# Performance work log

Hardware: AMD Instinct MI355X
Metric: run time of the kernel (lower is better)

## Reference

```python
import jax, jax.numpy as jnp
import numpy as np

B, N_HEADS, F_TOK = 8, 12, 768
GRID_H, GRID_W = 32, 32
N_TOK = 1 + GRID_H * GRID_W  # 1025 (readout token + patches)
F_HEAD = F_TOK // N_HEADS    # 64
NUM_DIST = (2 * GRID_H - 1) * (2 * GRID_W - 1) + 3  # 3972


def _build_relpos_index(gh, gw):
    # BEiT-style relative position index with 3 extra slots for the readout token
    coords = np.stack(np.meshgrid(np.arange(gh), np.arange(gw), indexing='ij'))  # (2, gh, gw)
    flat = coords.reshape(2, -1)                                                 # (2, gh*gw)
    rel = flat[:, :, None] - flat[:, None, :]                                    # (2, P, P)
    rel = rel.transpose(1, 2, 0).astype(np.int64)                                # (P, P, 2)
    rel[:, :, 0] += gh - 1
    rel[:, :, 1] += gw - 1
    rel[:, :, 0] *= 2 * gw - 1
    rpi = rel.sum(-1)                                                            # (P, P)
    n = 1 + gh * gw
    nd = (2 * gh - 1) * (2 * gw - 1) + 3
    idx = np.zeros((n, n), dtype=np.int32)
    idx[1:, 1:] = rpi
    idx[0, :] = nd - 3  # readout -> all
    idx[:, 0] = nd - 2  # all -> readout
    idx[0, 0] = nd - 1  # readout -> readout
    return idx


def setup_inputs() -> dict:
    key = jax.random.key(0)
    ks = jax.random.split(key, 7)
    tokens = jax.random.normal(ks[0], (B, N_TOK, F_TOK), dtype=jnp.float32)
    qkv_w = jax.random.normal(ks[1], (3 * F_TOK, F_TOK), dtype=jnp.float32) * 0.02
    q_bias = jax.random.normal(ks[2], (1, N_HEADS, 1, F_HEAD), dtype=jnp.float32) * 0.02
    v_bias = jax.random.normal(ks[3], (1, N_HEADS, 1, F_HEAD), dtype=jnp.float32) * 0.02
    relpos_table = jax.random.normal(ks[4], (NUM_DIST, N_HEADS), dtype=jnp.float32) * 0.02
    proj_w = jax.random.normal(ks[5], (F_TOK, F_TOK), dtype=jnp.float32) * 0.02
    proj_b = jax.random.normal(ks[6], (F_TOK,), dtype=jnp.float32) * 0.02
    relpos_index = jnp.asarray(_build_relpos_index(GRID_H, GRID_W))  # (N, N) int32
    return {
        'tokens': tokens, 'qkv_w': qkv_w, 'q_bias': q_bias, 'v_bias': v_bias,
        'relpos_table': relpos_table, 'proj_w': proj_w, 'proj_b': proj_b,
        'relpos_index': relpos_index, 'patch_h': GRID_H, 'patch_w': GRID_W,
    }


def reference(tokens, qkv_w, q_bias, v_bias, relpos_table, proj_w, proj_b,
              relpos_index, patch_h, patch_w):
    b, n, f_tok = tokens.shape
    # qkv projection (no bias): (B, N, 3F) -> (3, B, H, N, f)
    qkv = tokens @ qkv_w.T
    qkv = qkv.reshape(b, n, 3, N_HEADS, F_HEAD).transpose(2, 0, 3, 1, 4)
    q, k, v = qkv[0], qkv[1], qkv[2]
    q = (q + q_bias) * (F_HEAD ** -0.5)
    v = v + v_bias
    # attention scores: (B, H, N, N)
    attn = jnp.einsum('bhnf,bhmf->bhnm', q, k)
    # relative position bias gather: (N, N, H) -> (H, N, N)
    bias = relpos_table[relpos_index].transpose(2, 0, 1)
    attn = attn + bias[None]
    w = jax.nn.softmax(attn, axis=-1)
    out = jnp.einsum('bhnm,bhmf->bhnf', w, v)
    out = out.transpose(0, 2, 1, 3).reshape(b, n, N_HEADS * F_HEAD)
    return out @ proj_w.T + proj_b
```

## Files before the change

### kernel.cpp

```cpp
#include <hip/hip_runtime.h>

#define B_ 8
#define NH 12
#define NTOK 1025
#define FT 768
#define MROWS (B_*NTOK)
#define QPAD 1025
#define CH2 34
#define NQT 36
#define NTT 34
#define NRT18 18
#define NDIST 3972
#define LOG2E 1.44269504089f

typedef __bf16 bf16x8 __attribute__((ext_vector_type(8)));
typedef __bf16 bf16x2 __attribute__((ext_vector_type(2)));
typedef float floatx4 __attribute__((ext_vector_type(4)));
typedef float floatx16 __attribute__((ext_vector_type(16)));
typedef int intx4 __attribute__((ext_vector_type(4)));

__device__ __forceinline__ void async_ld16(const void* gp, void* lp) {
  __builtin_amdgcn_global_load_lds(
      (const __attribute__((address_space(1))) void*)gp,
      (__attribute__((address_space(3))) void*)lp, 16, 0, 0);
}

__global__ __launch_bounds__(256) void cvt_bf16(const float* __restrict__ src,
                                                __bf16* __restrict__ dst, int n4) {
  int i = blockIdx.x * 256 + threadIdx.x;
  if (i >= n4) return;
  float4 v = ((const float4*)src)[i];
  __bf16 o[4] = {(__bf16)v.x, (__bf16)v.y, (__bf16)v.z, (__bf16)v.w};
  *(uint2*)(dst + 4 * (size_t)i) = *(uint2*)o;
}

__global__ __launch_bounds__(256) void table_prep(const float* __restrict__ table,
                                                  __bf16* __restrict__ tableT) {
  int i = blockIdx.x * 256 + threadIdx.x;
  if (i >= NH * NDIST) return;
  int h = i / NDIST, d = i - h * NDIST;
  tableT[i] = (__bf16)(table[(size_t)d * NH + h] * LOG2E);
}

__global__ __launch_bounds__(256) void bias_gather_t(
    const int* __restrict__ idx, const __bf16* __restrict__ tableT,
    __bf16* __restrict__ Bb) {
  __shared__ int ids_l[32][33];
  const int qt = blockIdx.x, tt = blockIdx.y;
  const int t = threadIdx.x;
  {
    const int row = t >> 3, c4 = (t & 7) * 4;
    int qrow = qt * 32 + row; if (qrow > NTOK - 1) qrow = NTOK - 1;
    const int* src = idx + (size_t)qrow * NTOK;
#pragma unroll
    for (int j = 0; j < 4; ++j) {
      int token = tt * 32 + c4 + j; if (token > NTOK - 1) token = NTOK - 1;
      ids_l[row][c4 + j] = src[token];
    }
  }
  __syncthreads();
  const int lane = t & 63, w = t >> 6;
  const int l31 = lane & 31, hb = lane >> 5;
  int ids[16]; bool ok[16];
#pragma unroll
  for (int j = 0; j < 16; ++j) {
    const int col = (j & 3) + 8 * (j >> 2) + 4 * hb;
    ok[j] = tt * 32 + col < NTOK;
    ids[j] = ids_l[l31][col];
  }
#pragma unroll
  for (int g = 0; g < 3; ++g) {
    const int h = w + g * 4;
    const __bf16* tb = tableT + (size_t)h * NDIST;
    __bf16 v[16] __attribute__((aligned(16)));
#pragma unroll
    for (int j = 0; j < 16; ++j)
      v[j] = ok[j] ? tb[ids[j]] : (__bf16)(-1e30f);
    uint4* dst = (uint4*)(Bb + (((size_t)h * NQT + qt) * NTT + tt) * 1024 + lane * 16);
    dst[0] = ((uint4*)v)[0];
    dst[1] = ((uint4*)v)[1];
  }
}

__device__ __forceinline__ void gemm128_pipe(
    const __bf16* __restrict__ A, const __bf16* __restrict__ W,
    int am0, int n0, int amax, __bf16* At, __bf16* Bt, floatx4 acc[4][4]) {
  const int tid = threadIdx.x, wave = tid >> 6, lane = tid & 63;
  const int l = lane & 15, qd = lane >> 4;
  const int wr = wave >> 1, wc = wave & 1;
  const int srow = lane >> 2, sg = lane & 3;
  const int r0 = wave * 32 + srow, r1 = r0 + 16;
  int gm0 = am0 + r0; if (gm0 > amax) gm0 = amax;
  int gm1 = am0 + r1; if (gm1 > amax) gm1 = amax;
  const int sw0 = (sg ^ (r0 & 3)) * 8;
  const __bf16* gA0 = A + (size_t)gm0 * FT + sw0;
  const __bf16* gA1 = A + (size_t)gm1 * FT + sw0;
  const __bf16* gB0 = W + (size_t)(n0 + r0) * FT + sw0;
  const __bf16* gB1 = W + (size_t)(n0 + r1) * FT + sw0;
  const int woff = wave * 32 * 32;
  const int fsw = (qd ^ (l & 3)) * 8;

  auto issue = [&](int k, int buf) {
    __bf16* a = At + buf * 4096 + woff;
    __bf16* b = Bt + buf * 4096 + woff;
    async_ld16(gA0 + k * 32, a);
    async_ld16(gA1 + k * 32, a + 512);
    async_ld16(gB0 + k * 32, b);
    async_ld16(gB1 + k * 32, b + 512);
  };
  auto step = [&](int buf) {
    __builtin_amdgcn_s_barrier();
    const __bf16* ab = At + buf * 4096;
    const __bf16* bb = Bt + buf * 4096;
    bf16x8 aF[4], bF[4];
#pragma unroll
    for (int t = 0; t < 4; ++t)
      aF[t] = *(const bf16x8*)(ab + (wr * 64 + t * 16 + l) * 32 + fsw);
#pragma unroll
    for (int u = 0; u < 4; ++u)
      bF[u] = *(const bf16x8*)(bb + (wc * 64 + u * 16 + l) * 32 + fsw);
#pragma unroll
    for (int t = 0; t < 4; ++t)
#pragma unroll
      for (int u = 0; u < 4; ++u)
        acc[t][u] = __builtin_amdgcn_mfma_f32_16x16x32_bf16(aF[t], bF[u], acc[t][u], 0, 0, 0);
  };

  issue(0, 0);
  issue(1, 1);
  for (int k = 0; k < 24; ++k) {
    if (k + 2 < 24) {
      issue(k + 2, (k + 2) & 3);
      __builtin_amdgcn_s_waitcnt(0x0F78);
    } else if (k + 1 < 24) {
      __builtin_amdgcn_s_waitcnt(0x0F74);
    } else {
      __builtin_amdgcn_s_waitcnt(0x0F70);
    }
    step(k & 3);
  }
}

__global__ __launch_bounds__(256) void qkv_gemm128(
    const __bf16* __restrict__ tokens, const __bf16* __restrict__ qkvw,
    const float* __restrict__ qbias, const float* __restrict__ vbias,
    __bf16* __restrict__ Qb, __bf16* __restrict__ Kc, __bf16* __restrict__ Vc) {
  __shared__ __bf16 At[4 * 4096], Bt[4 * 4096];
  const int u0 = blockIdx.x;
  const int c = u0 & 7, q0 = u0 >> 3;
  const int mt = (q0 / 18) * 8 + c, ni = q0 % 18;
  const int b = mt / 9, ml = mt - b * 9;
  const int am0 = b * NTOK + ml * 128, amax = b * NTOK + 1024;
  const int n0 = ni * 128;
  const int tid = threadIdx.x, wave = tid >> 6, lane = tid & 63;
  const int l = lane & 15, qd = lane >> 4;
  const int wr = wave >> 1, wc = wave & 1;
  floatx4 acc[4][4];
#pragma unroll
  for (int t = 0; t < 4; ++t)
#pragma unroll
    for (int u = 0; u < 4; ++u) acc[t][u] = (floatx4){0.f, 0.f, 0.f, 0.f};
  gemm128_pipe(tokens, qkvw, am0, n0, amax, At, Bt, acc);

  const int which = ni / 6;
  const int nrem0 = (ni - which * 6) * 128;
  const bool full = (ml < 8);
  const int tokb = ml * 128 + wr * 64 + qd * 4;

  if (which == 0) {
#pragma unroll
    for (int u = 0; u < 4; ++u) {
      const int rem = nrem0 + wc * 64 + u * 16 + l;
      const int h = rem >> 6, f = rem & 63;
      const size_t bhq = ((size_t)(b * NH + h)) * QPAD;
      const float qb = qbias[h * 64 + f];
#pragma unroll
      for (int t = 0; t < 4; ++t) {
        const int tok = tokb + t * 16;
        if (full) {
          __bf16* qp = Qb + (bhq + tok) * 64 + f;
#pragma unroll
          for (int r = 0; r < 4; ++r)
            qp[r * 64] = (__bf16)((acc[t][u][r] + qb) * (0.125f * LOG2E));
        } else {
#pragma unroll
          for (int r = 0; r < 4; ++r)
            if (tok + r < NTOK)
              Qb[(bhq + tok + r) * 64 + f] = (__bf16)((acc[t][u][r] + qb) * (0.125f * LOG2E));
        }
      }
    }
  } else if (which == 1) {
#pragma unroll
    for (int u = 0; u < 4; ++u) {
      const int rem = nrem0 + wc * 64 + u * 16 + l;
      const int f = rem & 63;
      const size_t bhc = ((size_t)(b * NH + (rem >> 6))) * CH2;
      const int dgo = (f >> 3) * 256 + (f & 7);
#pragma unroll
      for (int t = 0; t < 4; ++t) {
        const int tok = tokb + t * 16;
        if (full) {
          const size_t base = (bhc + (tok >> 5)) * 2048 + dgo + (tok & 31) * 8;
#pragma unroll
          for (int r = 0; r < 4; ++r) Kc[base + r * 8] = (__bf16)acc[t][u][r];
        } else {
#pragma unroll
          for (int r = 0; r < 4; ++r) {
            const int tk = tok + r;
            if (tk < NTOK)
              Kc[(bhc + (tk >> 5)) * 2048 + (f >> 3) * 256 + (tk & 31) * 8 + (f & 7)] =
                  (__bf16)acc[t][u][r];
          }
        }
      }
    }
  } else {
#pragma unroll
    for (int u = 0; u < 4; ++u) {
      const int rem = nrem0 + wc * 64 + u * 16 + l;
      const int h = rem >> 6, f = rem & 63;
      const size_t bhc = ((size_t)(b * NH + h)) * CH2;
      const float vb = vbias[h * 64 + f];
#pragma unroll
      for (int t = 0; t < 4; ++t) {
        const int tok = tokb + t * 16;
        if (full) {
          __bf16 v4[4] __attribute__((aligned(8)));
#pragma unroll
          for (int r = 0; r < 4; ++r) v4[r] = (__bf16)(acc[t][u][r] + vb);
          const size_t e = (bhc + (tok >> 5)) * 2048 +
                           ((((tok >> 3) & 3) * 64 + f) << 3) + (tok & 7);
          *(uint2*)(Vc + e) = *(const uint2*)v4;
        } else {
#pragma unroll
          for (int r = 0; r < 4; ++r) {
            const int tk = tok + r;
            if (tk < NTOK)
              Vc[(bhc + (tk >> 5)) * 2048 + ((((tk >> 3) & 3) * 64 + f) << 3) + (tk & 7)] =
                  (__bf16)(acc[t][u][r] + vb);
          }
        }
      }
    }
  }
}

__global__ __launch_bounds__(256) void proj_gemm128(
    const __bf16* __restrict__ Ao, const __bf16* __restrict__ projw,
    const float* __restrict__ projb, float* __restrict__ out) {
  __shared__ __bf16 At[4 * 4096], Bt[4 * 4096];
  const int u0 = blockIdx.x;
  const int c = u0 & 7, q0 = u0 >> 3;
  const int mt = (q0 / 6) * 8 + c, ni = q0 % 6;
  const int b = mt / 9, ml = mt - b * 9;
  const int am0 = b * NTOK + ml * 128, amax = b * NTOK + 1024;
  const int n0 = ni * 128;
  const int tid = threadIdx.x, wave = tid >> 6, lane = tid & 63;
  const int l = lane & 15, qd = lane >> 4;
  const int wr = wave >> 1, wc = wave & 1;
  floatx4 acc[4][4];
#pragma unroll
  for (int t = 0; t < 4; ++t)
#pragma unroll
    for (int u = 0; u < 4; ++u) acc[t][u] = (floatx4){0.f, 0.f, 0.f, 0.f};
  gemm128_pipe(Ao, projw, am0, n0, amax, At, Bt, acc);

  const bool full = (ml < 8);
  const int tokb = ml * 128 + wr * 64 + qd * 4;
  const size_t rowb = (size_t)b * NTOK;
#pragma unroll
  for (int u = 0; u < 4; ++u) {
    const int gn = n0 + wc * 64 + u * 16 + l;
    const float pb = projb[gn];
#pragma unroll
    for (int t = 0; t < 4; ++t) {
      const int tok = tokb + t * 16;
      if (full) {
        float* op = out + (rowb + tok) * FT + gn;
#pragma unroll
        for (int r = 0; r < 4; ++r) op[(size_t)r * FT] = acc[t][u][r] + pb;
      } else {
#pragma unroll
        for (int r = 0; r < 4; ++r)
          if (tok + r < NTOK) out[(rowb + tok + r) * FT + gn] = acc[t][u][r] + pb;
      }
    }
  }
}

__global__ __launch_bounds__(128) void attn_flash(
    const __bf16* __restrict__ Qb, const __bf16* __restrict__ Kc,
    const __bf16* __restrict__ Vc, const __bf16* __restrict__ Bb,
    __bf16* __restrict__ Ao) {
  __shared__ __bf16 Kl[4][2048], Vl[4][2048];
  const int bh = blockIdx.x;
  const int rt = blockIdx.y;
  const int h = bh % NH, b = bh / NH;
  const int wave = threadIdx.x >> 6, lane = threadIdx.x & 63;
  const int l31 = lane & 31, hb = lane >> 5;
  const int qt = rt * 2 + wave;
  int qrow = qt * 32 + l31; if (qrow > NTOK - 1) qrow = NTOK - 1;

  bf16x8 qf[4];
  {
    const __bf16* Qp = Qb + ((size_t)bh * QPAD + qrow) * 64 + hb * 8;
#pragma unroll
    for (int d = 0; d < 4; ++d) qf[d] = *(const bf16x8*)(Qp + d * 16);
  }

  floatx16 o0, o1;
#pragma unroll
  for (int j = 0; j < 16; ++j) { o0[j] = 0.f; o1[j] = 0.f; }
  float lsum = 0.f;

  const __bf16* KVg = (wave ? Vc : Kc) + (size_t)bh * CH2 * 2048;
  const __bf16* Bg = Bb + ((size_t)h * NQT + qt) * NTT * 1024 + lane * 16;

  auto issue = [&](int c, int buf) {
    const __bf16* src = KVg + (size_t)c * 2048 + lane * 8;
    __bf16* dst = wave ? Vl[buf] : Kl[buf];
#pragma unroll
    for (int ii = 0; ii < 4; ++ii) async_ld16(src + ii * 512, dst + ii * 512);
  };

  bf16x8 bc0 = *(const bf16x8*)(Bg);
  bf16x8 bc1 = *(const bf16x8*)(Bg + 8);
  bf16x8 b10 = *(const bf16x8*)(Bg + 1024);
  bf16x8 b11 = *(const bf16x8*)(Bg + 1024 + 8);
  issue(0, 0);
  issue(1, 1);
  for (int c = 0; c < CH2; ++c) {
    bf16x8 b20 = b10, b21 = b11;
    if (c + 2 < CH2) {
      b20 = *(const bf16x8*)(Bg + (size_t)(c + 2) * 1024);
      b21 = *(const bf16x8*)(Bg + (size_t)(c + 2) * 1024 + 8);
      issue(c + 2, (c + 2) & 3);
      __builtin_amdgcn_s_waitcnt(0x0F7A);
    } else if (c + 1 < CH2) {
      __builtin_amdgcn_s_waitcnt(0x0F74);
    } else {
      __builtin_amdgcn_s_waitcnt(0x0F70);
    }
    __builtin_amdgcn_s_barrier();
    const __bf16* Kb = Kl[c & 3];
    const __bf16* Vb = Vl[c & 3];

    floatx16 st;
#pragma unroll
    for (int j = 0; j < 16; ++j) st[j] = 0.f;
#pragma unroll
    for (int dk = 0; dk < 4; ++dk) {
      bf16x8 a = *(const bf16x8*)(Kb + ((dk * 2 + hb) * 32 + l31) * 8);
      st = __builtin_amdgcn_mfma_f32_32x32x16_bf16(a, qf[dk], st, 0, 0, 0);
    }
    float e[16];
#pragma unroll
    for (int j = 0; j < 16; ++j) {
      const float bj = (float)(j < 8 ? bc0[j] : bc1[j - 8]);
      e[j] = __builtin_amdgcn_exp2f(st[j] + bj);
      lsum += e[j];
    }
    int pk[8];
#pragma unroll
    for (int j2 = 0; j2 < 8; ++j2) {
      bf16x2 pr = {(__bf16)e[2 * j2], (__bf16)e[2 * j2 + 1]};
      pk[j2] = __builtin_bit_cast(int, pr);
    }
#pragma unroll
    for (int ks = 0; ks < 2; ++ks) {
      const int r01a = pk[4 * ks + 0], r01b = pk[4 * ks + 1];
      const int r23a = pk[4 * ks + 2], r23b = pk[4 * ks + 3];
      const int t01a = __shfl_xor(r01a, 32), t01b = __shfl_xor(r01b, 32);
      const int t23a = __shfl_xor(r23a, 32), t23b = __shfl_xor(r23b, 32);
      intx4 fi;
      fi[0] = hb ? t23a : r01a;
      fi[1] = hb ? t23b : r01b;
      fi[2] = hb ? r23a : t01a;
      fi[3] = hb ? r23b : t01b;
      bf16x8 pb = __builtin_bit_cast(bf16x8, fi);
      bf16x8 va0 = *(const bf16x8*)(Vb + ((ks * 2 + hb) * 64 + l31) * 8);
      bf16x8 va1 = *(const bf16x8*)(Vb + ((ks * 2 + hb) * 64 + 32 + l31) * 8);
      o0 = __builtin_amdgcn_mfma_f32_32x32x16_bf16(va0, pb, o0, 0, 0, 0);
      o1 = __builtin_amdgcn_mfma_f32_32x32x16_bf16(va1, pb, o1, 0, 0, 0);
    }
    bc0 = b10; bc1 = b11; b10 = b20; b11 = b21;
  }

  const float ltot = lsum + __shfl_xor(lsum, 32);
  const float rinv = 1.0f / ltot;
  const int tok = rt * 64 + wave * 32 + l31;
  if (tok < NTOK) {
    __bf16* op = Ao + ((size_t)b * NTOK + tok) * FT + h * 64;
#pragma unroll
    for (int ft = 0; ft < 2; ++ft) {
#pragma unroll
      for (int jg = 0; jg < 4; ++jg) {
        const int f = ft * 32 + jg * 8 + hb * 4;
        __bf16 v4[4] __attribute__((aligned(8)));
#pragma unroll
        for (int q = 0; q < 4; ++q) {
          const float ov = ft ? o1[jg * 4 + q] : o0[jg * 4 + q];
          v4[q] = (__bf16)(ov * rinv);
        }
        *(uint2*)(op + f) = *(uint2*)v4;
      }
    }
  }
}

extern "C" void kernel_launch(void* const* d_in, const int* in_sizes, int n_in,
                              void* d_out, int out_size, void* d_ws, size_t ws_size,
                              hipStream_t stream) {
  (void)in_sizes; (void)n_in; (void)out_size; (void)ws_size;
  const float* tokens = (const float*)d_in[0];
  const float* qkvw   = (const float*)d_in[1];
  const float* qbias  = (const float*)d_in[2];
  const float* vbias  = (const float*)d_in[3];
  const float* table  = (const float*)d_in[4];
  const float* projw  = (const float*)d_in[5];
  const float* projb  = (const float*)d_in[6];
  const int*   rpidx  = (const int*)d_in[7];
  float* out = (float*)d_out;
  char* ws = (char*)d_ws;

  const size_t QBQ = (size_t)B_ * NH * QPAD * 64 * 2;
  const size_t KVB = (size_t)B_ * NH * CH2 * 2048 * 2;
  const size_t BBT = (size_t)NH * NQT * NTT * 1024 * 2;
  const size_t AOB = (size_t)MROWS * FT * 2;
  const size_t WQB = (size_t)3 * FT * FT * 2;
  const size_t WPB = (size_t)FT * FT * 2;
  __bf16* Qb = (__bf16*)(ws);
  __bf16* Kc = (__bf16*)(ws + QBQ);
  __bf16* Vc = (__bf16*)(ws + QBQ + KVB);
  __bf16* Bb = (__bf16*)(ws + QBQ + 2 * KVB);
  __bf16* Tb = (__bf16*)(ws + QBQ + 2 * KVB + BBT);
  __bf16* Ao = Tb;
  __bf16* Wq = (__bf16*)(ws + QBQ + 2 * KVB + BBT + AOB);
  __bf16* Wp = (__bf16*)(ws + QBQ + 2 * KVB + BBT + AOB + WQB);
  __bf16* Tt = (__bf16*)(ws + QBQ + 2 * KVB + BBT + AOB + WQB + WPB);

  cvt_bf16<<<(MROWS * FT / 4 + 255) / 256, 256, 0, stream>>>(tokens, Tb, MROWS * FT / 4);
  cvt_bf16<<<(3 * FT * FT / 4 + 255) / 256, 256, 0, stream>>>(qkvw, Wq, 3 * FT * FT / 4);
  cvt_bf16<<<(FT * FT / 4 + 255) / 256, 256, 0, stream>>>(projw, Wp, FT * FT / 4);
  table_prep<<<(NH * NDIST + 255) / 256, 256, 0, stream>>>(table, Tt);
  bias_gather_t<<<dim3(NQT, NTT), 256, 0, stream>>>(rpidx, Tt, Bb);
  qkv_gemm128<<<8 * 9 * 18, 256, 0, stream>>>(Tb, Wq, qbias, vbias, Qb, Kc, Vc);
  attn_flash<<<dim3(B_ * NH, NRT18), 128, 0, stream>>>(Qb, Kc, Vc, Bb, Ao);
  proj_gemm128<<<8 * 9 * 6, 256, 0, stream>>>(Ao, Wp, projb, out);
}
```

Measured before the change: 261.6 us.

## Deepen async LDS pipelines and widen attention blocks to four query tiles

The shared GEMM pipeline moves from a 4-slot ring with prefetch distance 2 to a 5-slot ring with prefetch distance 3. The attention kernel now runs 4 waves per block: each block covers four 32-row query tiles, and the K/V chunk loads are split across all four waves, so each loaded chunk serves twice as many queries. The attention loop keeps 5 LDS buffers in flight, hand-unrolls by two, and issues each bias load right after it is consumed, which removes the bias register rotation. The cost is more LDS per block, which may reduce occupancy, plus fragile hand-coded waitcnt values and buffer indices in the loop tail.

```diff
diff --git a/kernel.cpp b/kernel.cpp
--- a/kernel.cpp
+++ b/kernel.cpp
@@ -9,7 +9,6 @@
 #define CH2 34
 #define NQT 36
 #define NTT 34
-#define NRT18 18
 #define NDIST 3972
 #define LOG2E 1.44269504089f
 
@@ -128,16 +127,22 @@
 
   issue(0, 0);
   issue(1, 1);
+  issue(2, 2);
+  int b0 = 0, b3 = 3;
   for (int k = 0; k < 24; ++k) {
-    if (k + 2 < 24) {
-      issue(k + 2, (k + 2) & 3);
+    if (k < 21) {
+      issue(k + 3, b3);
+      __builtin_amdgcn_s_waitcnt(0x0F7C);
+    } else if (k == 21) {
       __builtin_amdgcn_s_waitcnt(0x0F78);
-    } else if (k + 1 < 24) {
+    } else if (k == 22) {
       __builtin_amdgcn_s_waitcnt(0x0F74);
     } else {
       __builtin_amdgcn_s_waitcnt(0x0F70);
     }
-    step(k & 3);
+    step(b0);
+    ++b0; if (b0 == 5) b0 = 0;
+    ++b3; if (b3 == 5) b3 = 0;
   }
 }
 
@@ -145,7 +150,7 @@
     const __bf16* __restrict__ tokens, const __bf16* __restrict__ qkvw,
     const float* __restrict__ qbias, const float* __restrict__ vbias,
     __bf16* __restrict__ Qb, __bf16* __restrict__ Kc, __bf16* __restrict__ Vc) {
-  __shared__ __bf16 At[4 * 4096], Bt[4 * 4096];
+  __shared__ __bf16 At[5 * 4096], Bt[5 * 4096];
   const int u0 = blockIdx.x;
   const int c = u0 & 7, q0 = u0 >> 3;
   const int mt = (q0 / 18) * 8 + c, ni = q0 % 18;
@@ -249,7 +254,7 @@
 __global__ __launch_bounds__(256) void proj_gemm128(
     const __bf16* __restrict__ Ao, const __bf16* __restrict__ projw,
     const float* __restrict__ projb, float* __restrict__ out) {
-  __shared__ __bf16 At[4 * 4096], Bt[4 * 4096];
+  __shared__ __bf16 At[5 * 4096], Bt[5 * 4096];
   const int u0 = blockIdx.x;
   const int c = u0 & 7, q0 = u0 >> 3;
   const int mt = (q0 / 6) * 8 + c, ni = q0 % 6;
@@ -289,17 +294,16 @@
   }
 }
 
-__global__ __launch_bounds__(128) void attn_flash(
+__global__ __launch_bounds__(256) void attn_flash(
     const __bf16* __restrict__ Qb, const __bf16* __restrict__ Kc,
     const __bf16* __restrict__ Vc, const __bf16* __restrict__ Bb,
     __bf16* __restrict__ Ao) {
-  __shared__ __bf16 Kl[4][2048], Vl[4][2048];
+  __shared__ __bf16 Kl[5][2048], Vl[5][2048];
   const int bh = blockIdx.x;
-  const int rt = blockIdx.y;
   const int h = bh % NH, b = bh / NH;
   const int wave = threadIdx.x >> 6, lane = threadIdx.x & 63;
   const int l31 = lane & 31, hb = lane >> 5;
-  const int qt = rt * 2 + wave;
+  const int qt = blockIdx.y * 4 + wave;
   int qrow = qt * 32 + l31; if (qrow > NTOK - 1) qrow = NTOK - 1;
 
   bf16x8 qf[4];
@@ -314,38 +318,22 @@
   for (int j = 0; j < 16; ++j) { o0[j] = 0.f; o1[j] = 0.f; }
   float lsum = 0.f;
 
-  const __bf16* KVg = (wave ? Vc : Kc) + (size_t)bh * CH2 * 2048;
+  const int sw = wave & 1;
+  const __bf16* Sg = ((wave < 2) ? Kc : Vc) + (size_t)bh * CH2 * 2048 +
+                     sw * 1024 + lane * 8;
+  __bf16* Sl0 = ((wave < 2) ? &Kl[0][0] : &Vl[0][0]) + sw * 1024;
   const __bf16* Bg = Bb + ((size_t)h * NQT + qt) * NTT * 1024 + lane * 16;
 
-  auto issue = [&](int c, int buf) {
-    const __bf16* src = KVg + (size_t)c * 2048 + lane * 8;
-    __bf16* dst = wave ? Vl[buf] : Kl[buf];
-#pragma unroll
-    for (int ii = 0; ii < 4; ++ii) async_ld16(src + ii * 512, dst + ii * 512);
+  auto issueS = [&](int c, int buf) {
+    const __bf16* src = Sg + (size_t)c * 2048;
+    __bf16* dst = Sl0 + buf * 2048;
+    async_ld16(src, dst);
+    async_ld16(src + 512, dst + 512);
   };
 
-  bf16x8 bc0 = *(const bf16x8*)(Bg);
-  bf16x8 bc1 = *(const bf16x8*)(Bg + 8);
-  bf16x8 b10 = *(const bf16x8*)(Bg + 1024);
-  bf16x8 b11 = *(const bf16x8*)(Bg + 1024 + 8);
-  issue(0, 0);
-  issue(1, 1);
-  for (int c = 0; c < CH2; ++c) {
-    bf16x8 b20 = b10, b21 = b11;
-    if (c + 2 < CH2) {
-      b20 = *(const bf16x8*)(Bg + (size_t)(c + 2) * 1024);
-      b21 = *(const bf16x8*)(Bg + (size_t)(c + 2) * 1024 + 8);
-      issue(c + 2, (c + 2) & 3);
-      __builtin_amdgcn_s_waitcnt(0x0F7A);
-    } else if (c + 1 < CH2) {
-      __builtin_amdgcn_s_waitcnt(0x0F74);
-    } else {
-      __builtin_amdgcn_s_waitcnt(0x0F70);
-    }
-    __builtin_amdgcn_s_barrier();
-    const __bf16* Kb = Kl[c & 3];
-    const __bf16* Vb = Vl[c & 3];
-
+  auto compute = [&](int buf, bf16x8 cb0, bf16x8 cb1) {
+    const __bf16* Kb = &Kl[buf][0];
+    const __bf16* Vb = &Vl[buf][0];
     floatx16 st;
 #pragma unroll
     for (int j = 0; j < 16; ++j) st[j] = 0.f;
@@ -357,7 +345,7 @@
     float e[16];
 #pragma unroll
     for (int j = 0; j < 16; ++j) {
-      const float bj = (float)(j < 8 ? bc0[j] : bc1[j - 8]);
+      const float bj = (float)(j < 8 ? cb0[j] : cb1[j - 8]);
       e[j] = __builtin_amdgcn_exp2f(st[j] + bj);
       lsum += e[j];
     }
@@ -384,12 +372,55 @@
       o0 = __builtin_amdgcn_mfma_f32_32x32x16_bf16(va0, pb, o0, 0, 0, 0);
       o1 = __builtin_amdgcn_mfma_f32_32x32x16_bf16(va1, pb, o1, 0, 0, 0);
     }
-    bc0 = b10; bc1 = b11; b10 = b20; b11 = b21;
-  }
+  };
+
+  issueS(0, 0);
+  bf16x8 bA0 = *(const bf16x8*)(Bg);
+  bf16x8 bA1 = *(const bf16x8*)(Bg + 8);
+  issueS(1, 1);
+  bf16x8 bB0 = *(const bf16x8*)(Bg + 1024);
+  bf16x8 bB1 = *(const bf16x8*)(Bg + 1024 + 8);
+  issueS(2, 2);
+
+  int bc = 0;
+  for (int ci = 0; ci < 15; ++ci) {
+    const int c = 2 * ci;
+    __builtin_amdgcn_s_waitcnt(0x0F76);
+    __builtin_amdgcn_s_barrier();
+    compute(bc, bA0, bA1);
+    bA0 = *(const bf16x8*)(Bg + (size_t)(c + 2) * 1024);
+    bA1 = *(const bf16x8*)(Bg + (size_t)(c + 2) * 1024 + 8);
+    { int b3 = bc + 3; if (b3 >= 5) b3 -= 5; issueS(c + 3, b3); }
+    int bc1 = bc + 1; if (bc1 == 5) bc1 = 0;
+    __builtin_amdgcn_s_waitcnt(0x0F76);
+    __builtin_amdgcn_s_barrier();
+    compute(bc1, bB0, bB1);
+    bB0 = *(const bf16x8*)(Bg + (size_t)(c + 3) * 1024);
+    bB1 = *(const bf16x8*)(Bg + (size_t)(c + 3) * 1024 + 8);
+    { int b4 = bc + 4; if (b4 >= 5) b4 -= 5; issueS(c + 4, b4); }
+    bc += 2; if (bc >= 5) bc -= 5;
+  }
+  __builtin_amdgcn_s_waitcnt(0x0F76);
+  __builtin_amdgcn_s_barrier();
+  compute(0, bA0, bA1);
+  bA0 = *(const bf16x8*)(Bg + (size_t)32 * 1024);
+  bA1 = *(const bf16x8*)(Bg + (size_t)32 * 1024 + 8);
+  issueS(33, 3);
+  __builtin_amdgcn_s_waitcnt(0x0F76);
+  __builtin_amdgcn_s_barrier();
+  compute(1, bB0, bB1);
+  bB0 = *(const bf16x8*)(Bg + (size_t)33 * 1024);
+  bB1 = *(const bf16x8*)(Bg + (size_t)33 * 1024 + 8);
+  __builtin_amdgcn_s_waitcnt(0x0F74);
+  __builtin_amdgcn_s_barrier();
+  compute(2, bA0, bA1);
+  __builtin_amdgcn_s_waitcnt(0x0F70);
+  __builtin_amdgcn_s_barrier();
+  compute(3, bB0, bB1);
 
   const float ltot = lsum + __shfl_xor(lsum, 32);
   const float rinv = 1.0f / ltot;
-  const int tok = rt * 64 + wave * 32 + l31;
+  const int tok = qt * 32 + l31;
   if (tok < NTOK) {
     __bf16* op = Ao + ((size_t)b * NTOK + tok) * FT + h * 64;
 #pragma unroll
@@ -446,6 +477,6 @@
   table_prep<<<(NH * NDIST + 255) / 256, 256, 0, stream>>>(table, Tt);
   bias_gather_t<<<dim3(NQT, NTT), 256, 0, stream>>>(rpidx, Tt, Bb);
   qkv_gemm128<<<8 * 9 * 18, 256, 0, stream>>>(Tb, Wq, qbias, vbias, Qb, Kc, Vc);
-  attn_flash<<<dim3(B_ * NH, NRT18), 128, 0, stream>>>(Qb, Kc, Vc, Bb, Ao);
+  attn_flash<<<dim3(B_ * NH, 9), 256, 0, stream>>>(Qb, Kc, Vc, Bb, Ao);
   proj_gemm128<<<8 * 9 * 6, 256, 0, stream>>>(Ao, Wp, projb, out);
 }
```

Result: faster. 245.7 us (-6.1%).
